# Performance work log

Measured on AMD Instinct MI355X. Metric: run time of the kernel, lower is better.

Reference implementation:

```python
import jax, jax.numpy as jnp
import numpy as np
import math

B, H, N, D = 2, 16, 2048, 64

def setup_inputs() -> dict:
    key = jax.random.key(0)
    kq, kk, kv, kb = jax.random.split(key, 4)
    return {
        "query": jax.random.normal(kq, (B, H, N, D), dtype=jnp.float32),
        "key": jax.random.normal(kk, (B, H, N, D), dtype=jnp.float32),
        "value": jax.random.normal(kv, (B, H, N, D), dtype=jnp.float32),
        "relative_position_bias": jax.random.normal(kb, (H, N, N), dtype=jnp.float32),
    }

def reference(query, key, value, relative_position_bias):
    d = query.shape[-1]
    # scores: [B,H,N,N]
    attn = jnp.einsum("bhnd,bhmd->bhnm", query, key) / jnp.sqrt(jnp.asarray(d, query.dtype))
    attn = attn + relative_position_bias[None]  # broadcast over batch
    attn = jax.nn.softmax(attn, axis=-1)
    # dropout p=0.0 -> identity
    output = jnp.einsum("bhnm,bhmd->bhnd", attn, value)
    return (output, attn)
```

## Files before the change

### kernel.cpp

```cpp
#include <hip/hip_runtime.h>
#include <cstdint>

#define BN 2
#define HN 16
#define NN 2048
#define DD 64
#define KT 64
#define NT (NN / KT)
#define LDP 72
#define LDF 68

typedef __attribute__((ext_vector_type(8))) short short8;
typedef __attribute__((ext_vector_type(4))) unsigned short ushort4v;
typedef __attribute__((ext_vector_type(4))) float float4v;

static __device__ __forceinline__ unsigned short f2bf(float f){
    uint32_t u = __builtin_bit_cast(uint32_t, f);
    u += 0x7FFFu + ((u >> 16) & 1u);
    return (unsigned short)(u >> 16);
}

static __device__ __forceinline__ float4v mfma_bf16(short8 a, short8 b, float4v c){
    return __builtin_amdgcn_mfma_f32_16x16x32_bf16(a, b, c, 0, 0, 0);
}

static __device__ __forceinline__ void barrier_lds(){
    asm volatile("s_waitcnt lgkmcnt(0)" ::: "memory");
    __builtin_amdgcn_s_barrier();
    asm volatile("" ::: "memory");
}

__launch_bounds__(256, 4)
__global__ void attn_fused_kernel(const float* __restrict__ Q,
                                  const float* __restrict__ K,
                                  const float* __restrict__ V,
                                  const float* __restrict__ Bias,
                                  float* __restrict__ Out){
    __shared__ unsigned short Kb[KT][LDP];
    __shared__ unsigned short Vt[DD][LDP];
    __shared__ float Pb[4][16][LDF];

    const int bid = blockIdx.x;
    const int b   = bid & 1;
    const int t2  = bid >> 1;
    const int rt  = t2 & 31;
    const int h   = t2 >> 5;

    const int tid = threadIdx.x;
    const int l   = tid & 63;
    const int w   = tid >> 6;
    const int lg  = l >> 4;
    const int ll  = l & 15;
    const int vc  = ll * 4;

    const int srow = tid >> 4;
    const int scol = (tid & 15) << 2;
    const int vsw  = ((tid >> 1) & 7) << 3;

    const int qw = rt * 64 + w * 16;
    const size_t bh = (size_t)(b * HN + h);
    const float* Qg = Q + (bh * NN + qw) * DD;
    const float* Kg = K + bh * NN * DD;
    const float* Vg = V + bh * NN * DD;
    const float* BgV = Bias + (size_t)h * NN * NN + (size_t)(qw + lg) * NN + vc;

    short8 qf[2];
    {
        const float* qrow = Qg + (size_t)ll * DD + lg * 8;
        #pragma unroll
        for(int ks = 0; ks < 2; ++ks){
            float4v f0 = *(const float4v*)(qrow + ks * 32);
            float4v f1 = *(const float4v*)(qrow + ks * 32 + 4);
            short8 s;
            s[0]=(short)f2bf(f0[0]); s[1]=(short)f2bf(f0[1]);
            s[2]=(short)f2bf(f0[2]); s[3]=(short)f2bf(f0[3]);
            s[4]=(short)f2bf(f1[0]); s[5]=(short)f2bf(f1[1]);
            s[6]=(short)f2bf(f1[2]); s[7]=(short)f2bf(f1[3]);
            qf[ks] = s;
        }
    }

    float lsum[4];
    #pragma unroll
    for(int r = 0; r < 4; ++r) lsum[r] = 0.f;

    float4v kreg[4], bv[4];
    #pragma unroll
    for(int i = 0; i < 4; ++i)
        kreg[i] = *(const float4v*)(Kg + (size_t)(srow + 16*i) * DD + scol);
    #pragma unroll
    for(int it = 0; it < 4; ++it)
        bv[it] = *(const float4v*)(BgV + (size_t)(it * 4) * NN);

    for(int ct = 0; ct < NT; ++ct){
        barrier_lds();
        #pragma unroll
        for(int i = 0; i < 4; ++i){
            ushort4v t;
            #pragma unroll
            for(int j = 0; j < 4; ++j) t[j] = f2bf(kreg[i][j]);
            *(ushort4v*)&Kb[srow + 16*i][scol] = t;
        }
        if(ct + 1 < NT){
            #pragma unroll
            for(int i = 0; i < 4; ++i)
                kreg[i] = *(const float4v*)(Kg + (size_t)((ct+1)*KT + srow + 16*i) * DD + scol);
        }
        barrier_lds();

        #pragma unroll
        for(int it = 0; it < 4; ++it)
            *(float4v*)&Pb[w][it*4 + lg][vc] = bv[it];
        if(ct + 1 < NT){
            #pragma unroll
            for(int it = 0; it < 4; ++it)
                bv[it] = *(const float4v*)(BgV + (size_t)(it * 4) * NN + (ct+1)*KT);
        }

        float4v acc[4];
        #pragma unroll
        for(int sub = 0; sub < 4; ++sub) acc[sub] = (float4v){0.f,0.f,0.f,0.f};
        __builtin_amdgcn_s_setprio(1);
        #pragma unroll
        for(int sub = 0; sub < 4; ++sub){
            short8 b0 = *(const short8*)&Kb[sub*16 + ll][lg*8];
            short8 b1 = *(const short8*)&Kb[sub*16 + ll][32 + lg*8];
            acc[sub] = mfma_bf16(qf[0], b0, acc[sub]);
            acc[sub] = mfma_bf16(qf[1], b1, acc[sub]);
        }
        __builtin_amdgcn_s_setprio(0);

        #pragma unroll
        for(int r = 0; r < 4; ++r){
            float e0 = __expf(acc[0][r] * 0.125f + Pb[w][lg*4+r][      ll]);
            float e1 = __expf(acc[1][r] * 0.125f + Pb[w][lg*4+r][16 +  ll]);
            float e2 = __expf(acc[2][r] * 0.125f + Pb[w][lg*4+r][32 +  ll]);
            float e3 = __expf(acc[3][r] * 0.125f + Pb[w][lg*4+r][48 +  ll]);
            lsum[r] += (e0 + e1) + (e2 + e3);
        }
    }

    float rl[4];
    #pragma unroll
    for(int r = 0; r < 4; ++r){
        #pragma unroll
        for(int d = 1; d < 16; d <<= 1) lsum[r] += __shfl_xor(lsum[r], d);
        rl[r] = 1.0f / lsum[r];
    }

    float4v oacc[4];
    #pragma unroll
    for(int ds = 0; ds < 4; ++ds) oacc[ds] = (float4v){0.f,0.f,0.f,0.f};

    float* attnW = Out + (size_t)BN*HN*NN*DD
                 + (bh * NN + qw + lg) * (size_t)NN + vc;

    float4v vreg[4];
    #pragma unroll
    for(int i = 0; i < 4; ++i){
        kreg[i] = *(const float4v*)(Kg + (size_t)(srow + 16*i) * DD + scol);
        vreg[i] = *(const float4v*)(Vg + (size_t)(srow + 16*i) * DD + scol);
    }
    #pragma unroll
    for(int it = 0; it < 4; ++it)
        bv[it] = *(const float4v*)(BgV + (size_t)(it * 4) * NN);

    for(int ct = 0; ct < NT; ++ct){
        barrier_lds();
        #pragma unroll
        for(int i = 0; i < 4; ++i){
            ushort4v t;
            #pragma unroll
            for(int j = 0; j < 4; ++j) t[j] = f2bf(kreg[i][j]);
            *(ushort4v*)&Kb[srow + 16*i][scol] = t;
            #pragma unroll
            for(int j = 0; j < 4; ++j)
                Vt[scol + j][(srow + 16*i) ^ vsw] = f2bf(vreg[i][j]);
        }
        if(ct + 1 < NT){
            #pragma unroll
            for(int i = 0; i < 4; ++i){
                kreg[i] = *(const float4v*)(Kg + (size_t)((ct+1)*KT + srow + 16*i) * DD + scol);
                vreg[i] = *(const float4v*)(Vg + (size_t)((ct+1)*KT + srow + 16*i) * DD + scol);
            }
        }
        barrier_lds();

        #pragma unroll
        for(int it = 0; it < 4; ++it)
            *(float4v*)&Pb[w][it*4 + lg][vc] = bv[it];
        if(ct + 1 < NT){
            #pragma unroll
            for(int it = 0; it < 4; ++it)
                bv[it] = *(const float4v*)(BgV + (size_t)(it * 4) * NN + (ct+1)*KT);
        }

        float4v acc[4];
        #pragma unroll
        for(int sub = 0; sub < 4; ++sub) acc[sub] = (float4v){0.f,0.f,0.f,0.f};
        __builtin_amdgcn_s_setprio(1);
        #pragma unroll
        for(int sub = 0; sub < 4; ++sub){
            short8 b0 = *(const short8*)&Kb[sub*16 + ll][lg*8];
            short8 b1 = *(const short8*)&Kb[sub*16 + ll][32 + lg*8];
            acc[sub] = mfma_bf16(qf[0], b0, acc[sub]);
            acc[sub] = mfma_bf16(qf[1], b1, acc[sub]);
        }
        __builtin_amdgcn_s_setprio(0);

        #pragma unroll
        for(int sub = 0; sub < 4; ++sub)
            #pragma unroll
            for(int r = 0; r < 4; ++r){
                float sv = acc[sub][r] * 0.125f + Pb[w][lg*4+r][sub*16+ll];
                Pb[w][lg*4+r][sub*16+ll] = __expf(sv) * rl[r];
            }

        short8 pf0, pf1;
        {
            float4v p0 = *(const float4v*)&Pb[w][ll][lg*8];
            float4v p1 = *(const float4v*)&Pb[w][ll][lg*8 + 4];
            float4v p2 = *(const float4v*)&Pb[w][ll][32 + lg*8];
            float4v p3 = *(const float4v*)&Pb[w][ll][32 + lg*8 + 4];
            #pragma unroll
            for(int j = 0; j < 4; ++j){
                pf0[j]   = (short)f2bf(p0[j]);
                pf0[4+j] = (short)f2bf(p1[j]);
                pf1[j]   = (short)f2bf(p2[j]);
                pf1[4+j] = (short)f2bf(p3[j]);
            }
        }

        #pragma unroll
        for(int it = 0; it < 4; ++it){
            float4v pv = *(const float4v*)&Pb[w][it*4 + lg][vc];
            *(float4v*)(attnW + (size_t)(it*4) * NN + ct*KT) = pv;
        }

        __builtin_amdgcn_s_setprio(1);
        #pragma unroll
        for(int ds = 0; ds < 4; ++ds){
            const int rsw = (2*ds + (ll >> 3)) << 3;
            short8 v0 = *(const short8*)&Vt[ds*16 + ll][(lg*8) ^ rsw];
            short8 v1 = *(const short8*)&Vt[ds*16 + ll][(32 + lg*8) ^ rsw];
            oacc[ds] = mfma_bf16(pf0, v0, oacc[ds]);
            oacc[ds] = mfma_bf16(pf1, v1, oacc[ds]);
        }
        __builtin_amdgcn_s_setprio(0);
    }

    float* outG = Out + (bh * NN + qw) * (size_t)DD;
    #pragma unroll
    for(int ds = 0; ds < 4; ++ds)
        #pragma unroll
        for(int r = 0; r < 4; ++r)
            outG[(size_t)(lg*4 + r) * DD + ds*16 + ll] = oacc[ds][r];
}

extern "C" void kernel_launch(void* const* d_in, const int* in_sizes, int n_in,
                              void* d_out, int out_size, void* d_ws, size_t ws_size,
                              hipStream_t stream) {
    const float* q    = (const float*)d_in[0];
    const float* k    = (const float*)d_in[1];
    const float* v    = (const float*)d_in[2];
    const float* bias = (const float*)d_in[3];
    float* out = (float*)d_out;

    dim3 grid(BN * HN * (NN / 64));
    dim3 block(256);
    hipLaunchKernelGGL(attn_fused_kernel, grid, block, 0, stream, q, k, v, bias, out);
}
```

Before: 335.1 us.

## Use hardware packed bf16 conversion and remap blocks to group heads per XCD

Replaces the software round-to-nearest-even float-to-bf16 routine with the v_cvt_pk_bf16_f32 instruction, converting two floats per instruction for the Q, K, V and P fragments. This removes several integer ALU ops per element in the inner loops. It also remaps blockIdx so that blocks sharing a slot (blockIdx mod 8, likely one XCD under round-robin dispatch) cover contiguous head and row-tile ranges, aiming to improve L2 reuse of K, V and bias. The asm conversion may differ from the software rounding for NaN, and the block mapping assumes the hardware dispatch order.

New measurement: 324.3 us. 3.2% less time.

```diff
diff --git a/kernel.cpp b/kernel.cpp
--- a/kernel.cpp
+++ b/kernel.cpp
@@ -11,13 +11,17 @@
 #define LDF 68
 
 typedef __attribute__((ext_vector_type(8))) short short8;
-typedef __attribute__((ext_vector_type(4))) unsigned short ushort4v;
+typedef __attribute__((ext_vector_type(2))) uint32_t uint2v;
+typedef __attribute__((ext_vector_type(4))) uint32_t uint4v;
 typedef __attribute__((ext_vector_type(4))) float float4v;
 
-static __device__ __forceinline__ unsigned short f2bf(float f){
-    uint32_t u = __builtin_bit_cast(uint32_t, f);
-    u += 0x7FFFu + ((u >> 16) & 1u);
-    return (unsigned short)(u >> 16);
+static __device__ __forceinline__ uint32_t cvt_pk_bf16(float a, float b){
+    uint32_t r;
+    asm("v_cvt_pk_bf16_f32 %0, %1, %2" : "=v"(r) : "v"(a), "v"(b));
+    return r;
+}
+static __device__ __forceinline__ unsigned short f2bf1(float a){
+    return (unsigned short)(cvt_pk_bf16(a, a) & 0xffffu);
 }
 
 static __device__ __forceinline__ float4v mfma_bf16(short8 a, short8 b, float4v c){
@@ -40,11 +44,13 @@
     __shared__ unsigned short Vt[DD][LDP];
     __shared__ float Pb[4][16][LDF];
 
-    const int bid = blockIdx.x;
-    const int b   = bid & 1;
-    const int t2  = bid >> 1;
-    const int rt  = t2 & 31;
-    const int h   = t2 >> 5;
+    const int raw  = blockIdx.x;
+    const int slot = raw & 7;
+    const int idx  = raw >> 3;
+    const int b    = idx & 1;
+    const int ghr  = slot * 64 + (idx >> 1);
+    const int h    = ghr >> 5;
+    const int rt   = ghr & 31;
 
     const int tid = threadIdx.x;
     const int l   = tid & 63;
@@ -71,12 +77,12 @@
         for(int ks = 0; ks < 2; ++ks){
             float4v f0 = *(const float4v*)(qrow + ks * 32);
             float4v f1 = *(const float4v*)(qrow + ks * 32 + 4);
-            short8 s;
-            s[0]=(short)f2bf(f0[0]); s[1]=(short)f2bf(f0[1]);
-            s[2]=(short)f2bf(f0[2]); s[3]=(short)f2bf(f0[3]);
-            s[4]=(short)f2bf(f1[0]); s[5]=(short)f2bf(f1[1]);
-            s[6]=(short)f2bf(f1[2]); s[7]=(short)f2bf(f1[3]);
-            qf[ks] = s;
+            uint4v u;
+            u[0] = cvt_pk_bf16(f0[0], f0[1]);
+            u[1] = cvt_pk_bf16(f0[2], f0[3]);
+            u[2] = cvt_pk_bf16(f1[0], f1[1]);
+            u[3] = cvt_pk_bf16(f1[2], f1[3]);
+            qf[ks] = __builtin_bit_cast(short8, u);
         }
     }
 
@@ -96,10 +102,9 @@
         barrier_lds();
         #pragma unroll
         for(int i = 0; i < 4; ++i){
-            ushort4v t;
-            #pragma unroll
-            for(int j = 0; j < 4; ++j) t[j] = f2bf(kreg[i][j]);
-            *(ushort4v*)&Kb[srow + 16*i][scol] = t;
+            uint2v t = { cvt_pk_bf16(kreg[i][0], kreg[i][1]),
+                         cvt_pk_bf16(kreg[i][2], kreg[i][3]) };
+            *(uint2v*)&Kb[srow + 16*i][scol] = t;
         }
         if(ct + 1 < NT){
             #pragma unroll
@@ -169,13 +174,12 @@
         barrier_lds();
         #pragma unroll
         for(int i = 0; i < 4; ++i){
-            ushort4v t;
-            #pragma unroll
-            for(int j = 0; j < 4; ++j) t[j] = f2bf(kreg[i][j]);
-            *(ushort4v*)&Kb[srow + 16*i][scol] = t;
+            uint2v t = { cvt_pk_bf16(kreg[i][0], kreg[i][1]),
+                         cvt_pk_bf16(kreg[i][2], kreg[i][3]) };
+            *(uint2v*)&Kb[srow + 16*i][scol] = t;
             #pragma unroll
             for(int j = 0; j < 4; ++j)
-                Vt[scol + j][(srow + 16*i) ^ vsw] = f2bf(vreg[i][j]);
+                Vt[scol + j][(srow + 16*i) ^ vsw] = f2bf1(vreg[i][j]);
         }
         if(ct + 1 < NT){
             #pragma unroll
@@ -222,13 +226,17 @@
             float4v p1 = *(const float4v*)&Pb[w][ll][lg*8 + 4];
             float4v p2 = *(const float4v*)&Pb[w][ll][32 + lg*8];
             float4v p3 = *(const float4v*)&Pb[w][ll][32 + lg*8 + 4];
-            #pragma unroll
-            for(int j = 0; j < 4; ++j){
-                pf0[j]   = (short)f2bf(p0[j]);
-                pf0[4+j] = (short)f2bf(p1[j]);
-                pf1[j]   = (short)f2bf(p2[j]);
-                pf1[4+j] = (short)f2bf(p3[j]);
-            }
+            uint4v u0, u1;
+            u0[0] = cvt_pk_bf16(p0[0], p0[1]);
+            u0[1] = cvt_pk_bf16(p0[2], p0[3]);
+            u0[2] = cvt_pk_bf16(p1[0], p1[1]);
+            u0[3] = cvt_pk_bf16(p1[2], p1[3]);
+            u1[0] = cvt_pk_bf16(p2[0], p2[1]);
+            u1[1] = cvt_pk_bf16(p2[2], p2[3]);
+            u1[2] = cvt_pk_bf16(p3[0], p3[1]);
+            u1[3] = cvt_pk_bf16(p3[2], p3[3]);
+            pf0 = __builtin_bit_cast(short8, u0);
+            pf1 = __builtin_bit_cast(short8, u1);
         }
 
         #pragma unroll
```
